# Kernel optimization log

Measured on AMD Instinct MI355X. Metric: run time of the kernel, lower is better.

The kernel has to match this reference:

```python
import jax, jax.numpy as jnp
import numpy as np
from functools import partial

CONF_THR = 0.25
IOU_THR = 0.4
MAX_DET = 100
NMS_TOPK = 4096  # static candidate pool for JIT-safe NMS (>> MAX_DET)
N_ANCHORS = 120000
N_CLASSES = 80


def setup_inputs() -> dict:
    key = jax.random.key(0)
    k1, = jax.random.split(key, 1)
    # raw YOLOv5 head output: [1, N, 4(xywh) + 1(obj) + C(class probs)]
    prediction = jax.random.uniform(k1, (1, N_ANCHORS, 5 + N_CLASSES), dtype=jnp.float32)
    image_size = jnp.array([960, 1280], dtype=jnp.int64)  # original (h, w)
    input_size = jnp.array([480, 640], dtype=jnp.int64)   # network input (h, w)
    return {"prediction": prediction, "image_size": image_size, "input_size": input_size}


def _pairwise_iou(boxes):
    # boxes: [K, 4] xyxy -> [K, K] IoU
    x1, y1, x2, y2 = boxes[:, 0], boxes[:, 1], boxes[:, 2], boxes[:, 3]
    area = jnp.maximum(x2 - x1, 0.0) * jnp.maximum(y2 - y1, 0.0)
    ix1 = jnp.maximum(x1[:, None], x1[None, :])
    iy1 = jnp.maximum(y1[:, None], y1[None, :])
    ix2 = jnp.minimum(x2[:, None], x2[None, :])
    iy2 = jnp.minimum(y2[:, None], y2[None, :])
    inter = jnp.maximum(ix2 - ix1, 0.0) * jnp.maximum(iy2 - iy1, 0.0)
    union = area[:, None] + area[None, :] - inter
    return inter / jnp.maximum(union, 1e-9)


def _forward(prediction, image_size, input_size):
    det = prediction[0]                      # [N, 5+C]
    xy, wh = det[:, :2], det[:, 2:4]
    obj = det[:, 4]
    probs = det[:, 5:]                       # [N, C]
    clf = jnp.max(probs, axis=-1)
    labels = jnp.argmax(probs, axis=-1)
    scores = obj * clf
    boxes = jnp.concatenate([xy - wh * 0.5, xy + wh * 0.5], axis=-1)  # xywh -> xyxy

    valid = scores > CONF_THR
    masked_scores = jnp.where(valid, scores, -jnp.inf)
    # static top-K candidate pool, sorted by descending score (greedy NMS order)
    top_scores, top_idx = jax.lax.top_k(masked_scores, NMS_TOPK)
    cand_boxes = boxes[top_idx]              # [K, 4]
    cand_labels = labels[top_idx]
    cand_probs = probs[top_idx]              # [K, C]
    cand_valid = valid[top_idx]

    # class-batched NMS: offset boxes per class so boxes of different classes never overlap
    max_coord = jnp.max(jnp.where(cand_valid[:, None], cand_boxes, 0.0)) + 1.0
    off_boxes = cand_boxes + (cand_labels.astype(cand_boxes.dtype) * max_coord)[:, None]
    iou = _pairwise_iou(off_boxes)           # [K, K]

    K = NMS_TOPK
    idx = jnp.arange(K)

    def body(i, keep):
        suppress = keep[i] & (iou[i] > IOU_THR) & (idx > i)
        return keep & ~suppress

    keep = jax.lax.fori_loop(0, K, body, cand_valid)

    # take the MAX_DET highest-scoring kept boxes (candidates already score-sorted)
    sel_scores = jnp.where(keep, top_scores, -jnp.inf)
    fin_scores, fin_idx = jax.lax.top_k(sel_scores, MAX_DET)
    fin_valid = keep[fin_idx]
    fb = cand_boxes[fin_idx]                 # [MAX_DET, 4] xyxy, input-size coords
    fprobs = cand_probs[fin_idx]             # [MAX_DET, C]

    # rescale from input_size to image_size (undo letterbox), clip, then normalized xywh
    img = image_size.astype(fb.dtype)        # (h0, w0)
    inp = input_size.astype(fb.dtype)        # (h1, w1)
    gain = jnp.min(inp / img)
    pad = (inp - img * gain) * 0.5           # (pad_h, pad_w)
    x1 = jnp.clip((fb[:, 0] - pad[1]) / gain, 0.0, img[1])
    y1 = jnp.clip((fb[:, 1] - pad[0]) / gain, 0.0, img[0])
    x2 = jnp.clip((fb[:, 2] - pad[1]) / gain, 0.0, img[1])
    y2 = jnp.clip((fb[:, 3] - pad[0]) / gain, 0.0, img[0])
    h, w = img[0], img[1]
    out_boxes = jnp.stack([
        (x1 + x2) * 0.5 / w,
        (y1 + y2) * 0.5 / h,
        (x2 - x1) / w,
        (y2 - y1) / h,
    ], axis=-1)                               # [MAX_DET, 4]

    m = fin_valid.astype(out_boxes.dtype)[:, None]
    out_boxes = out_boxes * m                 # zero padded slots
    out_scores = jnp.where(fin_valid, fin_scores, 0.0)[:, None]
    out_probs = fprobs * m
    return out_boxes, out_scores, out_probs


def reference(prediction, image_size, input_size):
    return _forward(prediction, image_size, input_size)
```

## Files before the change

kernel.cpp:

```cpp
#include <hip/hip_runtime.h>
#include <math.h>

#define N_ANCH 120000
#define N_CLS  80
#define TOPK   4096
#define MAXDET 100
#define CONF   0.25f
#define IOUT   0.4f
#define KEYCAP 30720

__device__ __forceinline__ unsigned f2ord(float f) {
    unsigned u = __float_as_uint(f);
    return (u & 0x80000000u) ? ~u : (u | 0x80000000u);
}
__device__ __forceinline__ float ord2f(unsigned o) {
    unsigned u = (o & 0x80000000u) ? (o & 0x7FFFFFFFu) : ~o;
    return __uint_as_float(u);
}
__device__ __forceinline__ unsigned long long shflx64(unsigned long long v, int m) {
    unsigned lo = (unsigned)__shfl_xor((int)(unsigned)v, m, 64);
    unsigned hi = (unsigned)__shfl_xor((int)(unsigned)(v >> 32), m, 64);
    return ((unsigned long long)hi << 32) | lo;
}
#define ORD_NEGINF 0x007FFFFFu
#define BMAP(b) ((((b) & 0xFFu) << 8) | ((unsigned)(b) >> 8))

__global__ __launch_bounds__(1024) void k_zero(unsigned* hist, unsigned* meta) {
    int i = blockIdx.x * 1024 + threadIdx.x;
    if (i < 65536) hist[i] = 0u;
    if (i < 64) meta[i] = 0u;
}

__global__ __launch_bounds__(256) void k_decode(const float* __restrict__ pred,
                                                unsigned* __restrict__ ord,
                                                int* __restrict__ lab,
                                                float4* __restrict__ box,
                                                unsigned* __restrict__ hist) {
    int wv = threadIdx.x >> 6, lane = threadIdx.x & 63;
    int a = blockIdx.x * 4 + wv;
    if (a >= N_ANCH) return;
    const float* p = pred + (long)a * 85;
    float v0 = p[lane];
    float v1 = (lane < 21) ? p[64 + lane] : 0.f;
    unsigned long long k0 = 0ull, k1 = 0ull;
    if (lane >= 5)
        k0 = ((unsigned long long)__float_as_uint(v0) << 32) | (0xFFFFFFFFu - (unsigned)(lane - 5));
    if (lane < 21)
        k1 = ((unsigned long long)__float_as_uint(v1) << 32) | (0xFFFFFFFFu - (unsigned)(59 + lane));
    unsigned long long key = k0 > k1 ? k0 : k1;
#pragma unroll
    for (int off = 1; off < 64; off <<= 1) {
        unsigned long long o = shflx64(key, off);
        if (o > key) key = o;
    }
    float best = __uint_as_float((unsigned)(key >> 32));
    int bl = (int)(0xFFFFFFFFu - (unsigned)(key & 0xFFFFFFFFu));
    float x = __shfl(v0, 0, 64), y = __shfl(v0, 1, 64);
    float w = __shfl(v0, 2, 64), h = __shfl(v0, 3, 64);
    float obj = __shfl(v0, 4, 64);
    if (lane == 0) {
        float sc = obj * best;
        bool valid = sc > CONF;
        float m = valid ? sc : -INFINITY;
        float hw = w * 0.5f, hh = h * 0.5f;
        float4 b;
        b.x = x - hw; b.y = y - hh; b.z = x + hw; b.w = y + hh;
        unsigned o = f2ord(m);
        ord[a] = o;
        lab[a] = bl;
        box[a] = b;
        if (valid) atomicAdd(&hist[BMAP(o >> 16)], 1u);
    }
}

__global__ __launch_bounds__(1024) void k_unperm(const unsigned* __restrict__ hist,
                                                 unsigned* __restrict__ cnt,
                                                 unsigned* __restrict__ chunkSum) {
    int b = blockIdx.x * 1024 + threadIdx.x;
    unsigned v = hist[BMAP(b)];
    cnt[b] = v;
    unsigned s = v;
#pragma unroll
    for (int off = 1; off < 64; off <<= 1) s += (unsigned)__shfl_xor((int)s, off, 64);
    if ((threadIdx.x & 63) == 0) chunkSum[b >> 6] = s;
}

__global__ __launch_bounds__(1024) void k_select0(const unsigned* __restrict__ cnt,
                                                  const unsigned* __restrict__ chunkSum,
                                                  unsigned* meta) {
    __shared__ unsigned part[1024];
    int t = threadIdx.x;
    part[t] = chunkSum[t];
    __syncthreads();
    for (int off = 1; off < 1024; off <<= 1) {
        unsigned v = (t + off < 1024) ? part[t + off] : 0u;
        __syncthreads();
        part[t] += v;
        __syncthreads();
    }
    unsigned incl = part[t];
    unsigned after = (t + 1 < 1024) ? part[t + 1] : 0u;
    if (after < (unsigned)TOPK && incl >= (unsigned)TOPK) {
        int base = t * 64;
        unsigned c64[64];
#pragma unroll
        for (int i = 0; i < 64; ++i) c64[i] = cnt[base + i];
        unsigned run = after;
        for (int i = 63; i >= 0; --i) {
            unsigned c = c64[i];
            if (run + c >= (unsigned)TOPK) { meta[0] = (unsigned)(base + i); break; }
            run += c;
        }
    }
}

__global__ __launch_bounds__(256) void k_compact(const unsigned* __restrict__ ord,
                                                 unsigned* meta,
                                                 unsigned long long* __restrict__ keys) {
    __shared__ unsigned wc[4];
    __shared__ unsigned sBase;
    int a = blockIdx.x * 256 + threadIdx.x;
    int lane = threadIdx.x & 63, wv = threadIdx.x >> 6;
    unsigned b1 = meta[0];
    unsigned o = (a < N_ANCH) ? ord[a] : 0u;
    bool isC = (a < N_ANCH) && ((o >> 16) >= b1);
    unsigned long long bal = __ballot(isC);
    if (lane == 0) wc[wv] = (unsigned)__popcll(bal);
    __syncthreads();
    if (threadIdx.x == 0) {
        unsigned tg = wc[0] + wc[1] + wc[2] + wc[3];
        sBase = tg ? atomicAdd(&meta[6], tg) : 0u;
    }
    __syncthreads();
    unsigned long long ltmask = (lane == 63) ? ~0ull >> 1 : (1ull << lane) - 1ull;
    if (isC) {
        unsigned p = sBase;
        for (int w = 0; w < wv; ++w) p += wc[w];
        p += (unsigned)__popcll(bal & ltmask);
        if (p < KEYCAP) keys[p] = ((unsigned long long)o << 32) | (unsigned)(~(unsigned)a);
    }
}

__global__ __launch_bounds__(1024) void k_rank(const unsigned long long* __restrict__ keys,
                                               const int* __restrict__ lab,
                                               const float4* __restrict__ box,
                                               int* __restrict__ cIdx,
                                               float* __restrict__ cScore,
                                               int* __restrict__ cLab,
                                               float4* __restrict__ cBox,
                                               unsigned* meta) {
    __shared__ float smax[16];
    int wv = threadIdx.x >> 6, lane = threadIdx.x & 63;
    unsigned K = meta[6];
    if (K > KEYCAP) K = KEYCAP;
    int nw = (int)((K + 63) >> 6);
    float mymax = 0.f;
    for (int i = blockIdx.x * 16 + wv; i < (int)K; i += 256 * 16) {
        unsigned long long ki = keys[i];
        unsigned cnt = 0;
#pragma unroll 8
        for (int k = 0; k < nw; ++k) {
            int idx = (k << 6) + lane;
            unsigned long long kv = (idx < (int)K) ? keys[idx] : 0ull;
            cnt += (kv > ki) ? 1u : 0u;
        }
#pragma unroll
        for (int off = 1; off < 64; off <<= 1) cnt += (unsigned)__shfl_xor((int)cnt, off, 64);
        if (lane == 0 && cnt < (unsigned)TOPK) {
            int r = (int)cnt;
            unsigned o = (unsigned)(ki >> 32);
            unsigned a = ~(unsigned)(ki & 0xFFFFFFFFu);
            float sc = ord2f(o);
            cIdx[r] = (int)a;
            cScore[r] = sc;
            cLab[r] = lab[a];
            float4 b = box[a];
            cBox[r] = b;
            if (sc > CONF)
                mymax = fmaxf(mymax, fmaxf(0.f, fmaxf(fmaxf(b.x, b.y), fmaxf(b.z, b.w))));
        }
    }
    if (lane == 0) smax[wv] = mymax;
    __syncthreads();
    if (threadIdx.x == 0) {
        float m = 0.f;
#pragma unroll
        for (int q = 0; q < 16; ++q) m = fmaxf(m, smax[q]);
        if (m > 0.f) atomicMax(&meta[8], __float_as_uint(m));
    }
}

__global__ __launch_bounds__(256) void k_mask(const float4* __restrict__ cBox,
                                              const int* __restrict__ cLab,
                                              const unsigned* __restrict__ meta,
                                              unsigned long long* __restrict__ M,
                                              unsigned long long* __restrict__ Diag) {
    int lane = threadIdx.x & 63;
    int i = blockIdx.x * 4 + (threadIdx.x >> 6);
    float mc = __uint_as_float(meta[8]) + 1.0f;
    float4 b = cBox[i];
    float offi = (float)cLab[i] * mc;
    float4 bi;
    bi.x = b.x + offi; bi.y = b.y + offi; bi.z = b.z + offi; bi.w = b.w + offi;
    float ai = fmaxf(bi.z - bi.x, 0.f) * fmaxf(bi.w - bi.y, 0.f);
    int w0 = i >> 6;
    unsigned long long myWord = 0ull;
    for (int jw = w0; jw < 64; ++jw) {
        int j = (jw << 6) + lane;
        float4 c = cBox[j];
        float offj = (float)cLab[j] * mc;
        float4 bj;
        bj.x = c.x + offj; bj.y = c.y + offj; bj.z = c.z + offj; bj.w = c.w + offj;
        float aj = fmaxf(bj.z - bj.x, 0.f) * fmaxf(bj.w - bj.y, 0.f);
        float ix1 = fmaxf(bi.x, bj.x), iy1 = fmaxf(bi.y, bj.y);
        float ix2 = fminf(bi.z, bj.z), iy2 = fminf(bi.w, bj.w);
        float inter = fmaxf(ix2 - ix1, 0.f) * fmaxf(iy2 - iy1, 0.f);
        float uni = ai + aj - inter;
        float iou = inter / fmaxf(uni, 1e-9f);
        bool bit = (j > i) & (iou > IOUT);
        unsigned long long word = __ballot(bit);
        if (lane == jw) myWord = word;
    }
    M[(long)i * 64 + lane] = myWord;
    if (lane == w0) Diag[i] = myWord;
}

__global__ __launch_bounds__(256) void k_nmsfinal(const unsigned long long* __restrict__ M,
                                                  const unsigned long long* __restrict__ Diag,
                                                  const float* __restrict__ cScore,
                                                  const float4* __restrict__ cBox,
                                                  const int* __restrict__ cIdx,
                                                  const float* __restrict__ pred,
                                                  const int* __restrict__ img,
                                                  const int* __restrict__ inp,
                                                  float* __restrict__ out,
                                                  int out_size) {
    __shared__ unsigned long long keepW[64];
    __shared__ int sel[MAXDET];
    __shared__ int nsel;
    int t = threadIdx.x;
    for (int i = t; i < out_size; i += 256) out[i] = 0.f;
    if (t == 0) nsel = 0;
    if (t < 64) {
        int lane = t;
        unsigned long long S = 0ull;
#pragma unroll 8
        for (int b = 0; b < 64; ++b) {
            float sc = cScore[(b << 6) + lane];
            unsigned long long bal = __ballot(!(sc > CONF));
            if (lane == b) S = bal;
        }
        unsigned long long d0 = Diag[lane];
        unsigned long long d1 = Diag[64 + lane];
        unsigned cnt = 0;
        int tstop = -1;
        unsigned long long ktStop = 0ull;
        for (int tt = 0; tt < 64; ++tt) {
            unsigned long long dcur = d0;
            d0 = d1;
            if (tt + 2 < 64) d1 = Diag[(tt + 2) * 64 + lane];
            unsigned long long s_tile =
                ((unsigned long long)(unsigned)__builtin_amdgcn_readlane((int)(unsigned)(S >> 32), tt)
                 << 32) |
                (unsigned)__builtin_amdgcn_readlane((int)(unsigned)S, tt);
#pragma unroll
            for (int b = 0; b < 64; ++b) {
                unsigned rl = (unsigned)__builtin_amdgcn_readlane((int)(unsigned)dcur, b);
                unsigned rh = (unsigned)__builtin_amdgcn_readlane((int)(unsigned)(dcur >> 32), b);
                unsigned long long row = ((unsigned long long)rh << 32) | rl;
                s_tile |= (((s_tile >> b) & 1ull) == 0ull) ? row : 0ull;
            }
            unsigned long long kt = ~s_tile;
            cnt += (unsigned)__popcll(kt);
            if (cnt >= MAXDET) { tstop = tt; ktStop = kt; break; }
            const unsigned long long* Mrow = M + (long)(tt << 6) * 64 + lane;
            unsigned long long a0 = 0, a1 = 0, a2 = 0, a3 = 0;
#pragma unroll
            for (int b = 0; b < 64; b += 4) {
                a0 |= Mrow[(long)(b + 0) * 64] & (0ull - ((kt >> (b + 0)) & 1ull));
                a1 |= Mrow[(long)(b + 1) * 64] & (0ull - ((kt >> (b + 1)) & 1ull));
                a2 |= Mrow[(long)(b + 2) * 64] & (0ull - ((kt >> (b + 2)) & 1ull));
                a3 |= Mrow[(long)(b + 3) * 64] & (0ull - ((kt >> (b + 3)) & 1ull));
            }
            S |= (a0 | a1) | (a2 | a3);
        }
        if (tstop >= 0) {
            keepW[lane] = (lane < tstop) ? ~S : (lane == tstop ? ktStop : 0ull);
        } else {
            keepW[lane] = ~S;
        }
    }
    __syncthreads();
    if (t < 64) {
        unsigned long long kw = keepW[t];
        int cnt = __popcll(kw);
        int incl = cnt;
        for (int off = 1; off < 64; off <<= 1) {
            int v = __shfl_up(incl, off);
            if (t >= off) incl += v;
        }
        int rk = incl - cnt;
        if (t == 63) nsel = (incl < MAXDET) ? incl : MAXDET;
        unsigned long long m = kw;
        while (m) {
            int b = __ffsll((unsigned long long)m) - 1;
            m &= m - 1;
            if (rk < MAXDET) sel[rk] = (t << 6) + b;
            ++rk;
        }
    }
    __syncthreads();
    int nk = nsel;
    int ih_i = img[0], iw_i = img[1];
    int nh_i = inp[0], nw_i = inp[1];
    if (iw_i == 0) iw_i = img[2];
    if (nw_i == 0) nw_i = inp[2];
    float ih = (float)ih_i, iw = (float)iw_i;
    float nh = (float)nh_i, nw = (float)nw_i;
    float gain = fminf(nh / ih, nw / iw);
    float pad0 = (nh - ih * gain) * 0.5f;
    float pad1 = (nw - iw * gain) * 0.5f;
    for (int o = t; o < nk; o += 256) {
        int k = sel[o];
        float4 b = cBox[k];
        float x1 = fminf(fmaxf((b.x - pad1) / gain, 0.f), iw);
        float y1 = fminf(fmaxf((b.y - pad0) / gain, 0.f), ih);
        float x2 = fminf(fmaxf((b.z - pad1) / gain, 0.f), iw);
        float y2 = fminf(fmaxf((b.w - pad0) / gain, 0.f), ih);
        out[o * 4 + 0] = (x1 + x2) * 0.5f / iw;
        out[o * 4 + 1] = (y1 + y2) * 0.5f / ih;
        out[o * 4 + 2] = (x2 - x1) / iw;
        out[o * 4 + 3] = (y2 - y1) / ih;
        out[4 * MAXDET + o] = cScore[k];
    }
    for (int p = t; p < nk * N_CLS; p += 256) {
        int o = p / N_CLS, c = p - o * N_CLS;
        int a = cIdx[sel[o]];
        out[5 * MAXDET + p] = pred[(long)a * 85 + 5 + c];
    }
}

extern "C" void kernel_launch(void* const* d_in, const int* in_sizes, int n_in,
                              void* d_out, int out_size, void* d_ws, size_t ws_size,
                              hipStream_t stream) {
    const float* pred = (const float*)d_in[0];
    const int* img = (const int*)d_in[1];
    const int* inp = (const int*)d_in[2];
    float* out = (float*)d_out;
    unsigned char* W = (unsigned char*)d_ws;

    unsigned* hist                = (unsigned*)(W + 0);
    unsigned* meta                = (unsigned*)(W + 262144);
    unsigned* ord                 = (unsigned*)(W + 262400);
    int* lab                      = (int*)(W + 742400);
    float4* box                   = (float4*)(W + 1222400);
    unsigned long long* keys      = (unsigned long long*)(W + 3142400);
    unsigned long long* M         = (unsigned long long*)(W + 3388160);
    unsigned long long* Diag      = (unsigned long long*)(W + 262400);
    int* cIdx                     = (int*)(W + 295168);
    float* cScore                 = (float*)(W + 311552);
    int* cLab                     = (int*)(W + 327936);
    float4* cBox                  = (float4*)(W + 344320);
    unsigned* cnt_lin             = (unsigned*)(W + 3388160);
    unsigned* chunkSum            = (unsigned*)(W + 3650304);

    int nb = (N_ANCH + 255) / 256;
    int nwb = (N_ANCH + 3) / 4;
    k_zero<<<64, 1024, 0, stream>>>(hist, meta);
    k_decode<<<nwb, 256, 0, stream>>>(pred, ord, lab, box, hist);
    k_unperm<<<64, 1024, 0, stream>>>(hist, cnt_lin, chunkSum);
    k_select0<<<1, 1024, 0, stream>>>(cnt_lin, chunkSum, meta);
    k_compact<<<nb, 256, 0, stream>>>(ord, meta, keys);
    k_rank<<<256, 1024, 0, stream>>>(keys, lab, box, cIdx, cScore, cLab, cBox, meta);
    k_mask<<<1024, 256, 0, stream>>>(cBox, cLab, meta, M, Diag);
    k_nmsfinal<<<1, 256, 0, stream>>>(M, Diag, cScore, cBox, cIdx, pred, img, inp, out, out_size);
}
```

Before: 115.9 us.

## Fuse all pipeline stages into one cooperative kernel with grid syncs

Replaces the eight separate kernel launches (zero, decode, histogram unpermute, threshold select, compaction, ranking, IoU mask, NMS/final) with a single cooperative kernel of 256 blocks x 1024 threads. Stages are separated by grid.sync() instead of kernel boundaries. The intent is to remove per-launch overhead and inter-kernel gaps. In exchange, decode now runs as a grid-stride loop over 4096 waves, so fewer memory requests are in flight during that stage, and every grid barrier adds its own sync cost. Cooperative launch also requires all blocks to be co-resident under the register limit for 1024-thread blocks.

```diff
diff --git a/kernel.cpp b/kernel.cpp
--- a/kernel.cpp
+++ b/kernel.cpp
@@ -1,5 +1,8 @@
 #include <hip/hip_runtime.h>
+#include <hip/hip_cooperative_groups.h>
 #include <math.h>
+
+namespace cg = cooperative_groups;
 
 #define N_ANCH 120000
 #define N_CLS  80
@@ -8,6 +11,7 @@
 #define CONF   0.25f
 #define IOUT   0.4f
 #define KEYCAP 30720
+#define NWAVE  4096
 
 __device__ __forceinline__ unsigned f2ord(float f) {
     unsigned u = __float_as_uint(f);
@@ -25,318 +29,311 @@
 #define ORD_NEGINF 0x007FFFFFu
 #define BMAP(b) ((((b) & 0xFFu) << 8) | ((unsigned)(b) >> 8))
 
-__global__ __launch_bounds__(1024) void k_zero(unsigned* hist, unsigned* meta) {
-    int i = blockIdx.x * 1024 + threadIdx.x;
-    if (i < 65536) hist[i] = 0u;
-    if (i < 64) meta[i] = 0u;
-}
-
-__global__ __launch_bounds__(256) void k_decode(const float* __restrict__ pred,
-                                                unsigned* __restrict__ ord,
-                                                int* __restrict__ lab,
-                                                float4* __restrict__ box,
-                                                unsigned* __restrict__ hist) {
-    int wv = threadIdx.x >> 6, lane = threadIdx.x & 63;
-    int a = blockIdx.x * 4 + wv;
-    if (a >= N_ANCH) return;
-    const float* p = pred + (long)a * 85;
-    float v0 = p[lane];
-    float v1 = (lane < 21) ? p[64 + lane] : 0.f;
-    unsigned long long k0 = 0ull, k1 = 0ull;
-    if (lane >= 5)
-        k0 = ((unsigned long long)__float_as_uint(v0) << 32) | (0xFFFFFFFFu - (unsigned)(lane - 5));
-    if (lane < 21)
-        k1 = ((unsigned long long)__float_as_uint(v1) << 32) | (0xFFFFFFFFu - (unsigned)(59 + lane));
-    unsigned long long key = k0 > k1 ? k0 : k1;
-#pragma unroll
-    for (int off = 1; off < 64; off <<= 1) {
-        unsigned long long o = shflx64(key, off);
-        if (o > key) key = o;
-    }
-    float best = __uint_as_float((unsigned)(key >> 32));
-    int bl = (int)(0xFFFFFFFFu - (unsigned)(key & 0xFFFFFFFFu));
-    float x = __shfl(v0, 0, 64), y = __shfl(v0, 1, 64);
-    float w = __shfl(v0, 2, 64), h = __shfl(v0, 3, 64);
-    float obj = __shfl(v0, 4, 64);
-    if (lane == 0) {
-        float sc = obj * best;
-        bool valid = sc > CONF;
-        float m = valid ? sc : -INFINITY;
-        float hw = w * 0.5f, hh = h * 0.5f;
-        float4 b;
-        b.x = x - hw; b.y = y - hh; b.z = x + hw; b.w = y + hh;
-        unsigned o = f2ord(m);
-        ord[a] = o;
-        lab[a] = bl;
-        box[a] = b;
-        if (valid) atomicAdd(&hist[BMAP(o >> 16)], 1u);
-    }
-}
-
-__global__ __launch_bounds__(1024) void k_unperm(const unsigned* __restrict__ hist,
-                                                 unsigned* __restrict__ cnt,
-                                                 unsigned* __restrict__ chunkSum) {
-    int b = blockIdx.x * 1024 + threadIdx.x;
-    unsigned v = hist[BMAP(b)];
-    cnt[b] = v;
-    unsigned s = v;
-#pragma unroll
-    for (int off = 1; off < 64; off <<= 1) s += (unsigned)__shfl_xor((int)s, off, 64);
-    if ((threadIdx.x & 63) == 0) chunkSum[b >> 6] = s;
-}
-
-__global__ __launch_bounds__(1024) void k_select0(const unsigned* __restrict__ cnt,
-                                                  const unsigned* __restrict__ chunkSum,
-                                                  unsigned* meta) {
-    __shared__ unsigned part[1024];
-    int t = threadIdx.x;
-    part[t] = chunkSum[t];
-    __syncthreads();
-    for (int off = 1; off < 1024; off <<= 1) {
-        unsigned v = (t + off < 1024) ? part[t + off] : 0u;
-        __syncthreads();
-        part[t] += v;
-        __syncthreads();
-    }
-    unsigned incl = part[t];
-    unsigned after = (t + 1 < 1024) ? part[t + 1] : 0u;
-    if (after < (unsigned)TOPK && incl >= (unsigned)TOPK) {
-        int base = t * 64;
-        unsigned c64[64];
-#pragma unroll
-        for (int i = 0; i < 64; ++i) c64[i] = cnt[base + i];
-        unsigned run = after;
-        for (int i = 63; i >= 0; --i) {
-            unsigned c = c64[i];
-            if (run + c >= (unsigned)TOPK) { meta[0] = (unsigned)(base + i); break; }
-            run += c;
-        }
-    }
-}
-
-__global__ __launch_bounds__(256) void k_compact(const unsigned* __restrict__ ord,
-                                                 unsigned* meta,
-                                                 unsigned long long* __restrict__ keys) {
-    __shared__ unsigned wc[4];
-    __shared__ unsigned sBase;
-    int a = blockIdx.x * 256 + threadIdx.x;
-    int lane = threadIdx.x & 63, wv = threadIdx.x >> 6;
-    unsigned b1 = meta[0];
-    unsigned o = (a < N_ANCH) ? ord[a] : 0u;
-    bool isC = (a < N_ANCH) && ((o >> 16) >= b1);
-    unsigned long long bal = __ballot(isC);
-    if (lane == 0) wc[wv] = (unsigned)__popcll(bal);
-    __syncthreads();
-    if (threadIdx.x == 0) {
-        unsigned tg = wc[0] + wc[1] + wc[2] + wc[3];
-        sBase = tg ? atomicAdd(&meta[6], tg) : 0u;
-    }
-    __syncthreads();
-    unsigned long long ltmask = (lane == 63) ? ~0ull >> 1 : (1ull << lane) - 1ull;
-    if (isC) {
-        unsigned p = sBase;
-        for (int w = 0; w < wv; ++w) p += wc[w];
-        p += (unsigned)__popcll(bal & ltmask);
-        if (p < KEYCAP) keys[p] = ((unsigned long long)o << 32) | (unsigned)(~(unsigned)a);
-    }
-}
-
-__global__ __launch_bounds__(1024) void k_rank(const unsigned long long* __restrict__ keys,
-                                               const int* __restrict__ lab,
-                                               const float4* __restrict__ box,
+__global__ __launch_bounds__(1024) void k_mega(const float* __restrict__ pred,
+                                               const int* __restrict__ img,
+                                               const int* __restrict__ inp,
+                                               float* __restrict__ out, int out_size,
+                                               unsigned* __restrict__ hist,
+                                               unsigned* __restrict__ meta,
+                                               unsigned* __restrict__ ord,
+                                               int* __restrict__ lab,
+                                               float4* __restrict__ box,
+                                               unsigned long long* __restrict__ keys,
+                                               unsigned long long* __restrict__ M,
+                                               unsigned long long* __restrict__ Diag,
                                                int* __restrict__ cIdx,
                                                float* __restrict__ cScore,
                                                int* __restrict__ cLab,
                                                float4* __restrict__ cBox,
-                                               unsigned* meta) {
+                                               unsigned* __restrict__ cnt,
+                                               unsigned* __restrict__ chunkSum) {
+    cg::grid_group grid = cg::this_grid();
+    __shared__ unsigned part[1024];
+    __shared__ unsigned wc[16];
+    __shared__ unsigned sBase;
     __shared__ float smax[16];
-    int wv = threadIdx.x >> 6, lane = threadIdx.x & 63;
-    unsigned K = meta[6];
-    if (K > KEYCAP) K = KEYCAP;
-    int nw = (int)((K + 63) >> 6);
-    float mymax = 0.f;
-    for (int i = blockIdx.x * 16 + wv; i < (int)K; i += 256 * 16) {
-        unsigned long long ki = keys[i];
-        unsigned cnt = 0;
-#pragma unroll 8
-        for (int k = 0; k < nw; ++k) {
-            int idx = (k << 6) + lane;
-            unsigned long long kv = (idx < (int)K) ? keys[idx] : 0ull;
-            cnt += (kv > ki) ? 1u : 0u;
-        }
-#pragma unroll
-        for (int off = 1; off < 64; off <<= 1) cnt += (unsigned)__shfl_xor((int)cnt, off, 64);
-        if (lane == 0 && cnt < (unsigned)TOPK) {
-            int r = (int)cnt;
-            unsigned o = (unsigned)(ki >> 32);
-            unsigned a = ~(unsigned)(ki & 0xFFFFFFFFu);
-            float sc = ord2f(o);
-            cIdx[r] = (int)a;
-            cScore[r] = sc;
-            cLab[r] = lab[a];
-            float4 b = box[a];
-            cBox[r] = b;
-            if (sc > CONF)
-                mymax = fmaxf(mymax, fmaxf(0.f, fmaxf(fmaxf(b.x, b.y), fmaxf(b.z, b.w))));
-        }
-    }
-    if (lane == 0) smax[wv] = mymax;
-    __syncthreads();
-    if (threadIdx.x == 0) {
-        float m = 0.f;
-#pragma unroll
-        for (int q = 0; q < 16; ++q) m = fmaxf(m, smax[q]);
-        if (m > 0.f) atomicMax(&meta[8], __float_as_uint(m));
-    }
-}
-
-__global__ __launch_bounds__(256) void k_mask(const float4* __restrict__ cBox,
-                                              const int* __restrict__ cLab,
-                                              const unsigned* __restrict__ meta,
-                                              unsigned long long* __restrict__ M,
-                                              unsigned long long* __restrict__ Diag) {
-    int lane = threadIdx.x & 63;
-    int i = blockIdx.x * 4 + (threadIdx.x >> 6);
-    float mc = __uint_as_float(meta[8]) + 1.0f;
-    float4 b = cBox[i];
-    float offi = (float)cLab[i] * mc;
-    float4 bi;
-    bi.x = b.x + offi; bi.y = b.y + offi; bi.z = b.z + offi; bi.w = b.w + offi;
-    float ai = fmaxf(bi.z - bi.x, 0.f) * fmaxf(bi.w - bi.y, 0.f);
-    int w0 = i >> 6;
-    unsigned long long myWord = 0ull;
-    for (int jw = w0; jw < 64; ++jw) {
-        int j = (jw << 6) + lane;
-        float4 c = cBox[j];
-        float offj = (float)cLab[j] * mc;
-        float4 bj;
-        bj.x = c.x + offj; bj.y = c.y + offj; bj.z = c.z + offj; bj.w = c.w + offj;
-        float aj = fmaxf(bj.z - bj.x, 0.f) * fmaxf(bj.w - bj.y, 0.f);
-        float ix1 = fmaxf(bi.x, bj.x), iy1 = fmaxf(bi.y, bj.y);
-        float ix2 = fminf(bi.z, bj.z), iy2 = fminf(bi.w, bj.w);
-        float inter = fmaxf(ix2 - ix1, 0.f) * fmaxf(iy2 - iy1, 0.f);
-        float uni = ai + aj - inter;
-        float iou = inter / fmaxf(uni, 1e-9f);
-        bool bit = (j > i) & (iou > IOUT);
-        unsigned long long word = __ballot(bit);
-        if (lane == jw) myWord = word;
-    }
-    M[(long)i * 64 + lane] = myWord;
-    if (lane == w0) Diag[i] = myWord;
-}
-
-__global__ __launch_bounds__(256) void k_nmsfinal(const unsigned long long* __restrict__ M,
-                                                  const unsigned long long* __restrict__ Diag,
-                                                  const float* __restrict__ cScore,
-                                                  const float4* __restrict__ cBox,
-                                                  const int* __restrict__ cIdx,
-                                                  const float* __restrict__ pred,
-                                                  const int* __restrict__ img,
-                                                  const int* __restrict__ inp,
-                                                  float* __restrict__ out,
-                                                  int out_size) {
     __shared__ unsigned long long keepW[64];
     __shared__ int sel[MAXDET];
     __shared__ int nsel;
+
     int t = threadIdx.x;
-    for (int i = t; i < out_size; i += 256) out[i] = 0.f;
-    if (t == 0) nsel = 0;
-    if (t < 64) {
-        int lane = t;
-        unsigned long long S = 0ull;
+    int gid = blockIdx.x * 1024 + t;
+    int wid = gid >> 6;
+    int lane = t & 63;
+    int wv = t >> 6;
+
+    if (gid < 65536) hist[gid] = 0u;
+    if (gid < 64) meta[gid] = 0u;
+    grid.sync();
+
+    for (int a = wid; a < N_ANCH; a += NWAVE) {
+        const float* p = pred + (long)a * 85;
+        float v0 = p[lane];
+        float v1 = (lane < 21) ? p[64 + lane] : 0.f;
+        unsigned long long k0 = 0ull, k1 = 0ull;
+        if (lane >= 5)
+            k0 = ((unsigned long long)__float_as_uint(v0) << 32) | (0xFFFFFFFFu - (unsigned)(lane - 5));
+        if (lane < 21)
+            k1 = ((unsigned long long)__float_as_uint(v1) << 32) | (0xFFFFFFFFu - (unsigned)(59 + lane));
+        unsigned long long key = k0 > k1 ? k0 : k1;
+#pragma unroll
+        for (int off = 1; off < 64; off <<= 1) {
+            unsigned long long o = shflx64(key, off);
+            if (o > key) key = o;
+        }
+        float best = __uint_as_float((unsigned)(key >> 32));
+        int bl = (int)(0xFFFFFFFFu - (unsigned)(key & 0xFFFFFFFFu));
+        float x = __shfl(v0, 0, 64), y = __shfl(v0, 1, 64);
+        float w = __shfl(v0, 2, 64), h = __shfl(v0, 3, 64);
+        float obj = __shfl(v0, 4, 64);
+        if (lane == 0) {
+            float sc = obj * best;
+            bool valid = sc > CONF;
+            float m = valid ? sc : -INFINITY;
+            float hw = w * 0.5f, hh = h * 0.5f;
+            float4 b;
+            b.x = x - hw; b.y = y - hh; b.z = x + hw; b.w = y + hh;
+            unsigned o = f2ord(m);
+            ord[a] = o;
+            lab[a] = bl;
+            box[a] = b;
+            if (valid) atomicAdd(&hist[BMAP(o >> 16)], 1u);
+        }
+    }
+    grid.sync();
+
+    if (gid < 65536) {
+        unsigned v = hist[BMAP(gid)];
+        cnt[gid] = v;
+        unsigned s = v;
+#pragma unroll
+        for (int off = 1; off < 64; off <<= 1) s += (unsigned)__shfl_xor((int)s, off, 64);
+        if (lane == 0) chunkSum[gid >> 6] = s;
+    }
+    grid.sync();
+
+    if (blockIdx.x == 0) {
+        part[t] = chunkSum[t];
+        __syncthreads();
+        for (int off = 1; off < 1024; off <<= 1) {
+            unsigned v = (t + off < 1024) ? part[t + off] : 0u;
+            __syncthreads();
+            part[t] += v;
+            __syncthreads();
+        }
+        unsigned incl = part[t];
+        unsigned after = (t + 1 < 1024) ? part[t + 1] : 0u;
+        if (after < (unsigned)TOPK && incl >= (unsigned)TOPK) {
+            int base = t * 64;
+            unsigned c64[64];
+#pragma unroll
+            for (int i = 0; i < 64; ++i) c64[i] = cnt[base + i];
+            unsigned run = after;
+            for (int i = 63; i >= 0; --i) {
+                unsigned c = c64[i];
+                if (run + c >= (unsigned)TOPK) { meta[0] = (unsigned)(base + i); break; }
+                run += c;
+            }
+        }
+    }
+    grid.sync();
+
+    {
+        int a = gid;
+        unsigned b1 = meta[0];
+        unsigned o = (a < N_ANCH) ? ord[a] : 0u;
+        bool isC = (a < N_ANCH) && ((o >> 16) >= b1);
+        unsigned long long bal = __ballot(isC);
+        if (lane == 0) wc[wv] = (unsigned)__popcll(bal);
+        __syncthreads();
+        if (t == 0) {
+            unsigned tg = 0;
+#pragma unroll
+            for (int q = 0; q < 16; ++q) tg += wc[q];
+            sBase = tg ? atomicAdd(&meta[6], tg) : 0u;
+        }
+        __syncthreads();
+        unsigned long long ltmask = (lane == 63) ? ~0ull >> 1 : (1ull << lane) - 1ull;
+        if (isC) {
+            unsigned p = sBase;
+            for (int w = 0; w < wv; ++w) p += wc[w];
+            p += (unsigned)__popcll(bal & ltmask);
+            if (p < KEYCAP) keys[p] = ((unsigned long long)o << 32) | (unsigned)(~(unsigned)a);
+        }
+    }
+    grid.sync();
+
+    {
+        unsigned K = meta[6];
+        if (K > KEYCAP) K = KEYCAP;
+        int nw = (int)((K + 63) >> 6);
+        float mymax = 0.f;
+        for (int i = blockIdx.x * 16 + wv; i < (int)K; i += NWAVE) {
+            unsigned long long ki = keys[i];
+            unsigned cntc = 0;
 #pragma unroll 8
-        for (int b = 0; b < 64; ++b) {
-            float sc = cScore[(b << 6) + lane];
-            unsigned long long bal = __ballot(!(sc > CONF));
-            if (lane == b) S = bal;
-        }
-        unsigned long long d0 = Diag[lane];
-        unsigned long long d1 = Diag[64 + lane];
-        unsigned cnt = 0;
-        int tstop = -1;
-        unsigned long long ktStop = 0ull;
-        for (int tt = 0; tt < 64; ++tt) {
-            unsigned long long dcur = d0;
-            d0 = d1;
-            if (tt + 2 < 64) d1 = Diag[(tt + 2) * 64 + lane];
-            unsigned long long s_tile =
-                ((unsigned long long)(unsigned)__builtin_amdgcn_readlane((int)(unsigned)(S >> 32), tt)
-                 << 32) |
-                (unsigned)__builtin_amdgcn_readlane((int)(unsigned)S, tt);
-#pragma unroll
+            for (int k = 0; k < nw; ++k) {
+                int idx = (k << 6) + lane;
+                unsigned long long kv = (idx < (int)K) ? keys[idx] : 0ull;
+                cntc += (kv > ki) ? 1u : 0u;
+            }
+#pragma unroll
+            for (int off = 1; off < 64; off <<= 1) cntc += (unsigned)__shfl_xor((int)cntc, off, 64);
+            if (lane == 0 && cntc < (unsigned)TOPK) {
+                int r = (int)cntc;
+                unsigned o = (unsigned)(ki >> 32);
+                unsigned a = ~(unsigned)(ki & 0xFFFFFFFFu);
+                float sc = ord2f(o);
+                cIdx[r] = (int)a;
+                cScore[r] = sc;
+                cLab[r] = lab[a];
+                float4 b = box[a];
+                cBox[r] = b;
+                if (sc > CONF)
+                    mymax = fmaxf(mymax, fmaxf(0.f, fmaxf(fmaxf(b.x, b.y), fmaxf(b.z, b.w))));
+            }
+        }
+        if (lane == 0) smax[wv] = mymax;
+        __syncthreads();
+        if (t == 0) {
+            float m = 0.f;
+#pragma unroll
+            for (int q = 0; q < 16; ++q) m = fmaxf(m, smax[q]);
+            if (m > 0.f) atomicMax(&meta[8], __float_as_uint(m));
+        }
+    }
+    grid.sync();
+
+    {
+        int i = wid;
+        float mc = __uint_as_float(meta[8]) + 1.0f;
+        float4 b = cBox[i];
+        float offi = (float)cLab[i] * mc;
+        float4 bi;
+        bi.x = b.x + offi; bi.y = b.y + offi; bi.z = b.z + offi; bi.w = b.w + offi;
+        float ai = fmaxf(bi.z - bi.x, 0.f) * fmaxf(bi.w - bi.y, 0.f);
+        int w0 = i >> 6;
+        unsigned long long myWord = 0ull;
+        for (int jw = w0; jw < 64; ++jw) {
+            int j = (jw << 6) + lane;
+            float4 c = cBox[j];
+            float offj = (float)cLab[j] * mc;
+            float4 bj;
+            bj.x = c.x + offj; bj.y = c.y + offj; bj.z = c.z + offj; bj.w = c.w + offj;
+            float aj = fmaxf(bj.z - bj.x, 0.f) * fmaxf(bj.w - bj.y, 0.f);
+            float ix1 = fmaxf(bi.x, bj.x), iy1 = fmaxf(bi.y, bj.y);
+            float ix2 = fminf(bi.z, bj.z), iy2 = fminf(bi.w, bj.w);
+            float inter = fmaxf(ix2 - ix1, 0.f) * fmaxf(iy2 - iy1, 0.f);
+            float uni = ai + aj - inter;
+            float iou = inter / fmaxf(uni, 1e-9f);
+            bool bit = (j > i) & (iou > IOUT);
+            unsigned long long word = __ballot(bit);
+            if (lane == jw) myWord = word;
+        }
+        M[(long)i * 64 + lane] = myWord;
+        if (lane == w0) Diag[i] = myWord;
+    }
+    grid.sync();
+
+    if (blockIdx.x == 0) {
+        for (int i = t; i < out_size; i += 1024) out[i] = 0.f;
+        if (t == 0) nsel = 0;
+        if (t < 64) {
+            unsigned long long S = 0ull;
+#pragma unroll 8
             for (int b = 0; b < 64; ++b) {
-                unsigned rl = (unsigned)__builtin_amdgcn_readlane((int)(unsigned)dcur, b);
-                unsigned rh = (unsigned)__builtin_amdgcn_readlane((int)(unsigned)(dcur >> 32), b);
-                unsigned long long row = ((unsigned long long)rh << 32) | rl;
-                s_tile |= (((s_tile >> b) & 1ull) == 0ull) ? row : 0ull;
-            }
-            unsigned long long kt = ~s_tile;
-            cnt += (unsigned)__popcll(kt);
-            if (cnt >= MAXDET) { tstop = tt; ktStop = kt; break; }
-            const unsigned long long* Mrow = M + (long)(tt << 6) * 64 + lane;
-            unsigned long long a0 = 0, a1 = 0, a2 = 0, a3 = 0;
-#pragma unroll
-            for (int b = 0; b < 64; b += 4) {
-                a0 |= Mrow[(long)(b + 0) * 64] & (0ull - ((kt >> (b + 0)) & 1ull));
-                a1 |= Mrow[(long)(b + 1) * 64] & (0ull - ((kt >> (b + 1)) & 1ull));
-                a2 |= Mrow[(long)(b + 2) * 64] & (0ull - ((kt >> (b + 2)) & 1ull));
-                a3 |= Mrow[(long)(b + 3) * 64] & (0ull - ((kt >> (b + 3)) & 1ull));
-            }
-            S |= (a0 | a1) | (a2 | a3);
-        }
-        if (tstop >= 0) {
-            keepW[lane] = (lane < tstop) ? ~S : (lane == tstop ? ktStop : 0ull);
-        } else {
-            keepW[lane] = ~S;
-        }
-    }
-    __syncthreads();
-    if (t < 64) {
-        unsigned long long kw = keepW[t];
-        int cnt = __popcll(kw);
-        int incl = cnt;
-        for (int off = 1; off < 64; off <<= 1) {
-            int v = __shfl_up(incl, off);
-            if (t >= off) incl += v;
-        }
-        int rk = incl - cnt;
-        if (t == 63) nsel = (incl < MAXDET) ? incl : MAXDET;
-        unsigned long long m = kw;
-        while (m) {
-            int b = __ffsll((unsigned long long)m) - 1;
-            m &= m - 1;
-            if (rk < MAXDET) sel[rk] = (t << 6) + b;
-            ++rk;
-        }
-    }
-    __syncthreads();
-    int nk = nsel;
-    int ih_i = img[0], iw_i = img[1];
-    int nh_i = inp[0], nw_i = inp[1];
-    if (iw_i == 0) iw_i = img[2];
-    if (nw_i == 0) nw_i = inp[2];
-    float ih = (float)ih_i, iw = (float)iw_i;
-    float nh = (float)nh_i, nw = (float)nw_i;
-    float gain = fminf(nh / ih, nw / iw);
-    float pad0 = (nh - ih * gain) * 0.5f;
-    float pad1 = (nw - iw * gain) * 0.5f;
-    for (int o = t; o < nk; o += 256) {
-        int k = sel[o];
-        float4 b = cBox[k];
-        float x1 = fminf(fmaxf((b.x - pad1) / gain, 0.f), iw);
-        float y1 = fminf(fmaxf((b.y - pad0) / gain, 0.f), ih);
-        float x2 = fminf(fmaxf((b.z - pad1) / gain, 0.f), iw);
-        float y2 = fminf(fmaxf((b.w - pad0) / gain, 0.f), ih);
-        out[o * 4 + 0] = (x1 + x2) * 0.5f / iw;
-        out[o * 4 + 1] = (y1 + y2) * 0.5f / ih;
-        out[o * 4 + 2] = (x2 - x1) / iw;
-        out[o * 4 + 3] = (y2 - y1) / ih;
-        out[4 * MAXDET + o] = cScore[k];
-    }
-    for (int p = t; p < nk * N_CLS; p += 256) {
-        int o = p / N_CLS, c = p - o * N_CLS;
-        int a = cIdx[sel[o]];
-        out[5 * MAXDET + p] = pred[(long)a * 85 + 5 + c];
+                float sc = cScore[(b << 6) + lane];
+                unsigned long long bal = __ballot(!(sc > CONF));
+                if (lane == b) S = bal;
+            }
+            unsigned long long d0 = Diag[lane];
+            unsigned long long d1 = Diag[64 + lane];
+            unsigned cntk = 0;
+            int tstop = -1;
+            unsigned long long ktStop = 0ull;
+            for (int tt = 0; tt < 64; ++tt) {
+                unsigned long long dcur = d0;
+                d0 = d1;
+                if (tt + 2 < 64) d1 = Diag[(tt + 2) * 64 + lane];
+                unsigned long long s_tile =
+                    ((unsigned long long)(unsigned)__builtin_amdgcn_readlane((int)(unsigned)(S >> 32), tt)
+                     << 32) |
+                    (unsigned)__builtin_amdgcn_readlane((int)(unsigned)S, tt);
+#pragma unroll
+                for (int b = 0; b < 64; ++b) {
+                    unsigned rl = (unsigned)__builtin_amdgcn_readlane((int)(unsigned)dcur, b);
+                    unsigned rh = (unsigned)__builtin_amdgcn_readlane((int)(unsigned)(dcur >> 32), b);
+                    unsigned long long row = ((unsigned long long)rh << 32) | rl;
+                    s_tile |= (((s_tile >> b) & 1ull) == 0ull) ? row : 0ull;
+                }
+                unsigned long long kt = ~s_tile;
+                cntk += (unsigned)__popcll(kt);
+                if (cntk >= MAXDET) { tstop = tt; ktStop = kt; break; }
+                const unsigned long long* Mrow = M + (long)(tt << 6) * 64 + lane;
+                unsigned long long a0 = 0, a1 = 0, a2 = 0, a3 = 0;
+#pragma unroll
+                for (int b = 0; b < 64; b += 4) {
+                    a0 |= Mrow[(long)(b + 0) * 64] & (0ull - ((kt >> (b + 0)) & 1ull));
+                    a1 |= Mrow[(long)(b + 1) * 64] & (0ull - ((kt >> (b + 1)) & 1ull));
+                    a2 |= Mrow[(long)(b + 2) * 64] & (0ull - ((kt >> (b + 2)) & 1ull));
+                    a3 |= Mrow[(long)(b + 3) * 64] & (0ull - ((kt >> (b + 3)) & 1ull));
+                }
+                S |= (a0 | a1) | (a2 | a3);
+            }
+            if (tstop >= 0) {
+                keepW[lane] = (lane < tstop) ? ~S : (lane == tstop ? ktStop : 0ull);
+            } else {
+                keepW[lane] = ~S;
+            }
+        }
+        __syncthreads();
+        if (t < 64) {
+            unsigned long long kw = keepW[t];
+            int cntb = __popcll(kw);
+            int incl = cntb;
+            for (int off = 1; off < 64; off <<= 1) {
+                int v = __shfl_up(incl, off);
+                if (t >= off) incl += v;
+            }
+            int rk = incl - cntb;
+            if (t == 63) nsel = (incl < MAXDET) ? incl : MAXDET;
+            unsigned long long m = kw;
+            while (m) {
+                int b = __ffsll((unsigned long long)m) - 1;
+                m &= m - 1;
+                if (rk < MAXDET) sel[rk] = (t << 6) + b;
+                ++rk;
+            }
+        }
+        __syncthreads();
+        int nk = nsel;
+        int ih_i = img[0], iw_i = img[1];
+        int nh_i = inp[0], nw_i = inp[1];
+        if (iw_i == 0) iw_i = img[2];
+        if (nw_i == 0) nw_i = inp[2];
+        float ih = (float)ih_i, iw = (float)iw_i;
+        float nh = (float)nh_i, nw = (float)nw_i;
+        float gain = fminf(nh / ih, nw / iw);
+        float pad0 = (nh - ih * gain) * 0.5f;
+        float pad1 = (nw - iw * gain) * 0.5f;
+        for (int o = t; o < nk; o += 1024) {
+            int k = sel[o];
+            float4 b = cBox[k];
+            float x1 = fminf(fmaxf((b.x - pad1) / gain, 0.f), iw);
+            float y1 = fminf(fmaxf((b.y - pad0) / gain, 0.f), ih);
+            float x2 = fminf(fmaxf((b.z - pad1) / gain, 0.f), iw);
+            float y2 = fminf(fmaxf((b.w - pad0) / gain, 0.f), ih);
+            out[o * 4 + 0] = (x1 + x2) * 0.5f / iw;
+            out[o * 4 + 1] = (y1 + y2) * 0.5f / ih;
+            out[o * 4 + 2] = (x2 - x1) / iw;
+            out[o * 4 + 3] = (y2 - y1) / ih;
+            out[4 * MAXDET + o] = cScore[k];
+        }
+        for (int p = t; p < nk * N_CLS; p += 1024) {
+            int o = p / N_CLS, c = p - o * N_CLS;
+            int a = cIdx[sel[o]];
+            out[5 * MAXDET + p] = pred[(long)a * 85 + 5 + c];
+        }
     }
 }
 
@@ -364,14 +361,11 @@
     unsigned* cnt_lin             = (unsigned*)(W + 3388160);
     unsigned* chunkSum            = (unsigned*)(W + 3650304);
 
-    int nb = (N_ANCH + 255) / 256;
-    int nwb = (N_ANCH + 3) / 4;
-    k_zero<<<64, 1024, 0, stream>>>(hist, meta);
-    k_decode<<<nwb, 256, 0, stream>>>(pred, ord, lab, box, hist);
-    k_unperm<<<64, 1024, 0, stream>>>(hist, cnt_lin, chunkSum);
-    k_select0<<<1, 1024, 0, stream>>>(cnt_lin, chunkSum, meta);
-    k_compact<<<nb, 256, 0, stream>>>(ord, meta, keys);
-    k_rank<<<256, 1024, 0, stream>>>(keys, lab, box, cIdx, cScore, cLab, cBox, meta);
-    k_mask<<<1024, 256, 0, stream>>>(cBox, cLab, meta, M, Diag);
-    k_nmsfinal<<<1, 256, 0, stream>>>(M, Diag, cScore, cBox, cIdx, pred, img, inp, out, out_size);
-}
+    void* args[] = {
+        (void*)&pred, (void*)&img, (void*)&inp, (void*)&out, (void*)&out_size,
+        (void*)&hist, (void*)&meta, (void*)&ord, (void*)&lab, (void*)&box,
+        (void*)&keys, (void*)&M, (void*)&Diag, (void*)&cIdx, (void*)&cScore,
+        (void*)&cLab, (void*)&cBox, (void*)&cnt_lin, (void*)&chunkSum
+    };
+    hipLaunchCooperativeKernel((void*)k_mega, dim3(256), dim3(1024), args, 0, stream);
+}
```

Result: slower. 284.8 us (+145.7%).

## Fuse select and NMS-final into predecessors via last-block atomic counters

Applied to the files above, without the earlier changes.

Merges the histogram unpermute kernel with the single-block threshold select, and the IoU mask kernel with the single-block greedy NMS finalization. In each case the last block to finish, detected through an atomic counter in meta, performs the serial tail. The zeroing kernel becomes a hipMemsetAsync over hist and meta. This removes kernel launches and inter-kernel gaps, at the cost of threadfences and a tail that runs on one block after the grid drains.

```diff
diff --git a/kernel.cpp b/kernel.cpp
--- a/kernel.cpp
+++ b/kernel.cpp
@@ -24,12 +24,6 @@
 }
 #define ORD_NEGINF 0x007FFFFFu
 #define BMAP(b) ((((b) & 0xFFu) << 8) | ((unsigned)(b) >> 8))
-
-__global__ __launch_bounds__(1024) void k_zero(unsigned* hist, unsigned* meta) {
-    int i = blockIdx.x * 1024 + threadIdx.x;
-    if (i < 65536) hist[i] = 0u;
-    if (i < 64) meta[i] = 0u;
-}
 
 __global__ __launch_bounds__(256) void k_decode(const float* __restrict__ pred,
                                                 unsigned* __restrict__ ord,
@@ -73,29 +67,35 @@
     }
 }
 
-__global__ __launch_bounds__(1024) void k_unperm(const unsigned* __restrict__ hist,
+__global__ __launch_bounds__(1024) void k_unpsel(const unsigned* __restrict__ hist,
                                                  unsigned* __restrict__ cnt,
-                                                 unsigned* __restrict__ chunkSum) {
-    int b = blockIdx.x * 1024 + threadIdx.x;
+                                                 unsigned* __restrict__ chunkSum,
+                                                 unsigned* __restrict__ meta) {
+    __shared__ unsigned part[1024];
+    __shared__ bool isLast;
+    int t = threadIdx.x;
+    int b = blockIdx.x * 1024 + t;
     unsigned v = hist[BMAP(b)];
     cnt[b] = v;
     unsigned s = v;
 #pragma unroll
     for (int off = 1; off < 64; off <<= 1) s += (unsigned)__shfl_xor((int)s, off, 64);
-    if ((threadIdx.x & 63) == 0) chunkSum[b >> 6] = s;
-}
-
-__global__ __launch_bounds__(1024) void k_select0(const unsigned* __restrict__ cnt,
-                                                  const unsigned* __restrict__ chunkSum,
-                                                  unsigned* meta) {
-    __shared__ unsigned part[1024];
-    int t = threadIdx.x;
+    if ((t & 63) == 0) chunkSum[b >> 6] = s;
+    __syncthreads();
+    if (t == 0) {
+        __threadfence();
+        unsigned done = atomicAdd(&meta[32], 1u);
+        isLast = (done == 63u);
+    }
+    __syncthreads();
+    if (!isLast) return;
+    __threadfence();
     part[t] = chunkSum[t];
     __syncthreads();
     for (int off = 1; off < 1024; off <<= 1) {
-        unsigned v = (t + off < 1024) ? part[t + off] : 0u;
+        unsigned pv = (t + off < 1024) ? part[t + off] : 0u;
         __syncthreads();
-        part[t] += v;
+        part[t] += pv;
         __syncthreads();
     }
     unsigned incl = part[t];
@@ -190,59 +190,65 @@
     }
 }
 
-__global__ __launch_bounds__(256) void k_mask(const float4* __restrict__ cBox,
-                                              const int* __restrict__ cLab,
-                                              const unsigned* __restrict__ meta,
-                                              unsigned long long* __restrict__ M,
-                                              unsigned long long* __restrict__ Diag) {
-    int lane = threadIdx.x & 63;
-    int i = blockIdx.x * 4 + (threadIdx.x >> 6);
-    float mc = __uint_as_float(meta[8]) + 1.0f;
-    float4 b = cBox[i];
-    float offi = (float)cLab[i] * mc;
-    float4 bi;
-    bi.x = b.x + offi; bi.y = b.y + offi; bi.z = b.z + offi; bi.w = b.w + offi;
-    float ai = fmaxf(bi.z - bi.x, 0.f) * fmaxf(bi.w - bi.y, 0.f);
-    int w0 = i >> 6;
-    unsigned long long myWord = 0ull;
-    for (int jw = w0; jw < 64; ++jw) {
-        int j = (jw << 6) + lane;
-        float4 c = cBox[j];
-        float offj = (float)cLab[j] * mc;
-        float4 bj;
-        bj.x = c.x + offj; bj.y = c.y + offj; bj.z = c.z + offj; bj.w = c.w + offj;
-        float aj = fmaxf(bj.z - bj.x, 0.f) * fmaxf(bj.w - bj.y, 0.f);
-        float ix1 = fmaxf(bi.x, bj.x), iy1 = fmaxf(bi.y, bj.y);
-        float ix2 = fminf(bi.z, bj.z), iy2 = fminf(bi.w, bj.w);
-        float inter = fmaxf(ix2 - ix1, 0.f) * fmaxf(iy2 - iy1, 0.f);
-        float uni = ai + aj - inter;
-        float iou = inter / fmaxf(uni, 1e-9f);
-        bool bit = (j > i) & (iou > IOUT);
-        unsigned long long word = __ballot(bit);
-        if (lane == jw) myWord = word;
-    }
-    M[(long)i * 64 + lane] = myWord;
-    if (lane == w0) Diag[i] = myWord;
-}
-
-__global__ __launch_bounds__(256) void k_nmsfinal(const unsigned long long* __restrict__ M,
-                                                  const unsigned long long* __restrict__ Diag,
-                                                  const float* __restrict__ cScore,
-                                                  const float4* __restrict__ cBox,
-                                                  const int* __restrict__ cIdx,
-                                                  const float* __restrict__ pred,
-                                                  const int* __restrict__ img,
-                                                  const int* __restrict__ inp,
-                                                  float* __restrict__ out,
-                                                  int out_size) {
+__global__ __launch_bounds__(256) void k_masknms(const float4* __restrict__ cBox,
+                                                 const int* __restrict__ cLab,
+                                                 unsigned* __restrict__ meta,
+                                                 unsigned long long* __restrict__ M,
+                                                 unsigned long long* __restrict__ Diag,
+                                                 const float* __restrict__ cScore,
+                                                 const int* __restrict__ cIdx,
+                                                 const float* __restrict__ pred,
+                                                 const int* __restrict__ img,
+                                                 const int* __restrict__ inp,
+                                                 float* __restrict__ out,
+                                                 int out_size) {
     __shared__ unsigned long long keepW[64];
     __shared__ int sel[MAXDET];
     __shared__ int nsel;
+    __shared__ bool isLast;
     int t = threadIdx.x;
+    int lane = t & 63;
+    {
+        int i = blockIdx.x * 4 + (t >> 6);
+        float mc = __uint_as_float(meta[8]) + 1.0f;
+        float4 b = cBox[i];
+        float offi = (float)cLab[i] * mc;
+        float4 bi;
+        bi.x = b.x + offi; bi.y = b.y + offi; bi.z = b.z + offi; bi.w = b.w + offi;
+        float ai = fmaxf(bi.z - bi.x, 0.f) * fmaxf(bi.w - bi.y, 0.f);
+        int w0 = i >> 6;
+        unsigned long long myWord = 0ull;
+        for (int jw = w0; jw < 64; ++jw) {
+            int j = (jw << 6) + lane;
+            float4 c = cBox[j];
+            float offj = (float)cLab[j] * mc;
+            float4 bj;
+            bj.x = c.x + offj; bj.y = c.y + offj; bj.z = c.z + offj; bj.w = c.w + offj;
+            float aj = fmaxf(bj.z - bj.x, 0.f) * fmaxf(bj.w - bj.y, 0.f);
+            float ix1 = fmaxf(bi.x, bj.x), iy1 = fmaxf(bi.y, bj.y);
+            float ix2 = fminf(bi.z, bj.z), iy2 = fminf(bi.w, bj.w);
+            float inter = fmaxf(ix2 - ix1, 0.f) * fmaxf(iy2 - iy1, 0.f);
+            float uni = ai + aj - inter;
+            float iou = inter / fmaxf(uni, 1e-9f);
+            bool bit = (j > i) & (iou > IOUT);
+            unsigned long long word = __ballot(bit);
+            if (lane == jw) myWord = word;
+        }
+        M[(long)i * 64 + lane] = myWord;
+        if (lane == w0) Diag[i] = myWord;
+    }
+    __syncthreads();
+    if (t == 0) {
+        __threadfence();
+        unsigned done = atomicAdd(&meta[33], 1u);
+        isLast = (done == 1023u);
+    }
+    __syncthreads();
+    if (!isLast) return;
+    __threadfence();
     for (int i = t; i < out_size; i += 256) out[i] = 0.f;
     if (t == 0) nsel = 0;
     if (t < 64) {
-        int lane = t;
         unsigned long long S = 0ull;
 #pragma unroll 8
         for (int b = 0; b < 64; ++b) {
@@ -252,7 +258,7 @@
         }
         unsigned long long d0 = Diag[lane];
         unsigned long long d1 = Diag[64 + lane];
-        unsigned cnt = 0;
+        unsigned cntk = 0;
         int tstop = -1;
         unsigned long long ktStop = 0ull;
         for (int tt = 0; tt < 64; ++tt) {
@@ -271,8 +277,8 @@
                 s_tile |= (((s_tile >> b) & 1ull) == 0ull) ? row : 0ull;
             }
             unsigned long long kt = ~s_tile;
-            cnt += (unsigned)__popcll(kt);
-            if (cnt >= MAXDET) { tstop = tt; ktStop = kt; break; }
+            cntk += (unsigned)__popcll(kt);
+            if (cntk >= MAXDET) { tstop = tt; ktStop = kt; break; }
             const unsigned long long* Mrow = M + (long)(tt << 6) * 64 + lane;
             unsigned long long a0 = 0, a1 = 0, a2 = 0, a3 = 0;
 #pragma unroll
@@ -293,13 +299,13 @@
     __syncthreads();
     if (t < 64) {
         unsigned long long kw = keepW[t];
-        int cnt = __popcll(kw);
-        int incl = cnt;
+        int cntb = __popcll(kw);
+        int incl = cntb;
         for (int off = 1; off < 64; off <<= 1) {
             int v = __shfl_up(incl, off);
             if (t >= off) incl += v;
         }
-        int rk = incl - cnt;
+        int rk = incl - cntb;
         if (t == 63) nsel = (incl < MAXDET) ? incl : MAXDET;
         unsigned long long m = kw;
         while (m) {
@@ -364,14 +370,14 @@
     unsigned* cnt_lin             = (unsigned*)(W + 3388160);
     unsigned* chunkSum            = (unsigned*)(W + 3650304);
 
+    hipMemsetAsync(W, 0, 262400, stream);
+
     int nb = (N_ANCH + 255) / 256;
     int nwb = (N_ANCH + 3) / 4;
-    k_zero<<<64, 1024, 0, stream>>>(hist, meta);
     k_decode<<<nwb, 256, 0, stream>>>(pred, ord, lab, box, hist);
-    k_unperm<<<64, 1024, 0, stream>>>(hist, cnt_lin, chunkSum);
-    k_select0<<<1, 1024, 0, stream>>>(cnt_lin, chunkSum, meta);
+    k_unpsel<<<64, 1024, 0, stream>>>(hist, cnt_lin, chunkSum, meta);
     k_compact<<<nb, 256, 0, stream>>>(ord, meta, keys);
     k_rank<<<256, 1024, 0, stream>>>(keys, lab, box, cIdx, cScore, cLab, cBox, meta);
-    k_mask<<<1024, 256, 0, stream>>>(cBox, cLab, meta, M, Diag);
-    k_nmsfinal<<<1, 256, 0, stream>>>(M, Diag, cScore, cBox, cIdx, pred, img, inp, out, out_size);
-}
+    k_masknms<<<1024, 256, 0, stream>>>(cBox, cLab, meta, M, Diag,
+                                        cScore, cIdx, pred, img, inp, out, out_size);
+}
```

New measurement: 136.9 us. 18.1% more time.
